# Kernel tuning notes

Measured on AMD Instinct MI355X. Metric: run time of the kernel, lower is better.

The kernel has to match this reference:

```python
import jax, jax.numpy as jnp
import numpy as np

N_NODES = 100000
N_EDGES = 1600000
NFEAT = 256
NHID = 128


def _l2_normalize(v, eps=1e-12):
    return v / (jnp.linalg.norm(v) + eps)


def setup_inputs() -> dict:
    key = jax.random.key(0)
    k1, k2, k3, k4 = jax.random.split(key, 4)
    x = jax.random.normal(k1, (N_NODES, NFEAT), dtype=jnp.float32)
    edge_index = jax.random.randint(k2, (2, N_EDGES), 0, N_NODES, dtype=jnp.int64)
    # GCNConv weight (glorot-ish scale), spectral-normalized at forward time
    W = jax.random.normal(k3, (NFEAT, NHID), dtype=jnp.float32) * 0.05
    bias = jnp.zeros((NHID,), dtype=jnp.float32)
    prelu_a = jnp.full((1,), 0.25, dtype=jnp.float32)  # nn.PReLU default slope
    u = _l2_normalize(jax.random.normal(k4, (NFEAT,), dtype=jnp.float32))
    return {"x": x, "edge_index": edge_index, "W": W, "bias": bias,
            "prelu_a": prelu_a, "u": u}


def reference(x, edge_index, W, bias, prelu_a, u):
    # --- spectral_norm: one power iteration (torch default n_power_iterations=1) ---
    v = _l2_normalize(W.T @ u)          # [NHID]
    u2 = _l2_normalize(W @ v)           # [NFEAT]
    sigma = u2 @ (W @ v)
    W_sn = W / sigma

    # --- GCNConv: linear transform, add self-loops, sym-normalize, scatter-add ---
    xw = x @ W_sn                       # [N, NHID]
    n = x.shape[0]
    loops = jnp.arange(n, dtype=edge_index.dtype)
    row = jnp.concatenate([edge_index[0], loops])  # sources
    col = jnp.concatenate([edge_index[1], loops])  # targets
    ones = jnp.ones(row.shape[0], dtype=x.dtype)
    deg = jax.ops.segment_sum(ones, col, num_segments=n)
    dinv = jnp.where(deg > 0, deg ** -0.5, 0.0)
    norm = dinv[row] * dinv[col]        # [E+N]
    msgs = norm[:, None] * xw[row]      # gather at sources
    out = jax.ops.segment_sum(msgs, col, num_segments=n) + bias

    # --- PReLU ---
    return jnp.where(out > 0, out, prelu_a * out)
```

## Files before the change

### kernel.cpp

```cpp
#include <hip/hip_runtime.h>

#define NFEAT 256
#define NHID  128

#define NBK   391
#define EPB   4096
#define NBLK  391

typedef __bf16 bf16x8 __attribute__((ext_vector_type(8)));
typedef __bf16 bf16x4 __attribute__((ext_vector_type(4)));
typedef float  f32x4  __attribute__((ext_vector_type(4)));

__global__ __launch_bounds__(256) void sigma_kernel(const float* __restrict__ W,
                                                    const float* __restrict__ u,
                                                    float* __restrict__ scal) {
    __shared__ float v[NHID];
    __shared__ float red[256];
    int tid = threadIdx.x;

    float t = 0.f;
    if (tid < NHID) {
        for (int i = 0; i < NFEAT; ++i) t += W[i * NHID + tid] * u[i];
    }
    red[tid] = (tid < NHID) ? t * t : 0.f;
    __syncthreads();
    for (int s = 128; s > 0; s >>= 1) {
        if (tid < s) red[tid] += red[tid + s];
        __syncthreads();
    }
    float nv = sqrtf(red[0]);
    float inv_nv = 1.f / (nv + 1e-12f);
    __syncthreads();
    if (tid < NHID) v[tid] = t * inv_nv;
    __syncthreads();

    float wv = 0.f;
    for (int j = 0; j < NHID; ++j) wv += W[tid * NHID + j] * v[j];
    red[tid] = wv * wv;
    __syncthreads();
    for (int s = 128; s > 0; s >>= 1) {
        if (tid < s) red[tid] += red[tid + s];
        __syncthreads();
    }
    if (tid == 0) {
        float n2  = red[0];
        float nwv = sqrtf(n2);
        float sigma = n2 / (nwv + 1e-12f);
        scal[0] = 1.f / sigma;
    }
}

__global__ __launch_bounds__(256) void wt_kernel(const float* __restrict__ W,
                                                 const float* __restrict__ scal,
                                                 __bf16* __restrict__ WT) {
    int idx = blockIdx.x * 256 + threadIdx.x;
    int c = idx >> 8;
    int r = idx & 255;
    WT[c * NFEAT + r] = (__bf16)(W[r * NHID + c] * scal[0]);
}

__global__ __launch_bounds__(256) void hist_kernel(const int* __restrict__ ecol,
                                                   int* __restrict__ blkhist, int E) {
    __shared__ int hist[NBK];
    int tid = threadIdx.x, b = blockIdx.x;
    for (int k = tid; k < NBK; k += 256) hist[k] = 0;
    __syncthreads();
    int e0 = b * EPB;
#pragma unroll
    for (int j = 0; j < 16; ++j) {
        int idx = e0 + j * 256 + tid;
        if (idx < E) atomicAdd(&hist[ecol[idx] >> 8], 1);
    }
    __syncthreads();
    for (int k = tid; k < NBK; k += 256) blkhist[k * NBLK + b] = hist[k];
}

__global__ __launch_bounds__(256) void scan_rows_kernel(int* __restrict__ blkhist,
                                                        int* __restrict__ btot) {
    int k = blockIdx.x * 4 + (threadIdx.x >> 6);
    int lane = threadIdx.x & 63;
    if (k >= NBK) return;
    int carry = 0;
    for (int c0 = 0; c0 < NBLK; c0 += 64) {
        int b = c0 + lane;
        int v = (b < NBLK) ? blkhist[k * NBLK + b] : 0;
        int orig = v;
#pragma unroll
        for (int d = 1; d < 64; d <<= 1) {
            int t = __shfl_up(v, (unsigned)d, 64);
            if (lane >= d) v += t;
        }
        if (b < NBLK) blkhist[k * NBLK + b] = carry + v - orig;
        carry += __shfl(v, 63, 64);
    }
    if (lane == 0) btot[k] = carry;
}

__global__ __launch_bounds__(512) void scan_buckets_kernel(const int* __restrict__ btot,
                                                           int* __restrict__ bbase) {
    __shared__ int s[512];
    int tid = threadIdx.x;
    int v = (tid < NBK) ? btot[tid] : 0;
    s[tid] = v;
    __syncthreads();
    int val = v;
    for (int off = 1; off < 512; off <<= 1) {
        int t = (tid >= off) ? s[tid - off] : 0;
        __syncthreads();
        val += t;
        s[tid] = val;
        __syncthreads();
    }
    if (tid <= NBK) bbase[tid] = val - v;
}

__global__ __launch_bounds__(512) void coarse_scatter_kernel(const int* __restrict__ erow,
                                                             const int* __restrict__ ecol,
                                                             const int* __restrict__ blkhist,
                                                             const int* __restrict__ bbase,
                                                             unsigned int* __restrict__ rbuf,
                                                             int E) {
    __shared__ unsigned int rec[EPB];
    __shared__ unsigned short bk[EPB];
    __shared__ int hist[NBK], sc[512], lbase[NBK], lfill[NBK], gb[NBK];
    int tid = threadIdx.x, b = blockIdx.x;
    for (int k = tid; k < NBK; k += 512) { hist[k] = 0; lfill[k] = 0; }
    __syncthreads();
    int e0 = b * EPB;
    unsigned int rv[8];
    int kv[8];
#pragma unroll
    for (int j = 0; j < 8; ++j) {
        int idx = e0 + j * 512 + tid;
        if (idx < E) {
            int c = ecol[idx];
            int s = erow[idx];
            int k = c >> 8;
            kv[j] = k;
            rv[j] = ((unsigned int)(c & 255) << 24) | (unsigned int)s;
            atomicAdd(&hist[k], 1);
        } else kv[j] = -1;
    }
    __syncthreads();
    int hv = (tid < NBK) ? hist[tid] : 0;
    sc[tid] = hv;
    __syncthreads();
    int val = hv;
    for (int off = 1; off < 512; off <<= 1) {
        int t = (tid >= off) ? sc[tid - off] : 0;
        __syncthreads();
        val += t;
        sc[tid] = val;
        __syncthreads();
    }
    if (tid < NBK) {
        lbase[tid] = val - hv;
        gb[tid] = bbase[tid] + blkhist[tid * NBLK + b];
    }
    __syncthreads();
#pragma unroll
    for (int j = 0; j < 8; ++j) {
        if (kv[j] >= 0) {
            int p = lbase[kv[j]] + atomicAdd(&lfill[kv[j]], 1);
            rec[p] = rv[j];
            bk[p] = (unsigned short)kv[j];
        }
    }
    __syncthreads();
    int nval = E - e0;
    if (nval > EPB) nval = EPB;
    for (int p = tid; p < nval; p += 512) {
        int k = bk[p];
        rbuf[gb[k] + (p - lbase[k])] = rec[p];
    }
}

__global__ __launch_bounds__(256) void fine_kernel(const unsigned int* __restrict__ rbuf,
                                                   const int* __restrict__ bbase,
                                                   int* __restrict__ base_g,
                                                   int* __restrict__ cnt_g,
                                                   float* __restrict__ dinv,
                                                   int* __restrict__ ebuf, int n) {
    __shared__ int cnt[256], lb[256], lf[256], sc[256];
    int tid = threadIdx.x, k = blockIdx.x;
    int seg0 = bbase[k], seg1 = bbase[k + 1];
    cnt[tid] = 0;
    lf[tid] = 0;
    __syncthreads();
    for (int j = seg0 + tid; j < seg1; j += 256)
        atomicAdd(&cnt[rbuf[j] >> 24], 1);
    __syncthreads();
    int cv = cnt[tid];
    sc[tid] = cv;
    __syncthreads();
    int val = cv;
    for (int off = 1; off < 256; off <<= 1) {
        int t = (tid >= off) ? sc[tid - off] : 0;
        __syncthreads();
        val += t;
        sc[tid] = val;
        __syncthreads();
    }
    lb[tid] = val - cv;
    __syncthreads();
    int node = k * 256 + tid;
    if (node < n) {
        base_g[node] = seg0 + lb[tid];
        cnt_g[node] = cv;
        dinv[node] = rsqrtf((float)cv + 1.f);
    }
    for (int j = seg0 + tid; j < seg1; j += 256) {
        unsigned int r = rbuf[j];
        int dl = r >> 24;
        int p = seg0 + lb[dl] + atomicAdd(&lf[dl], 1);
        ebuf[p] = (int)(r & 0xFFFFFFu);
    }
}

__global__ __launch_bounds__(256) void gemm_mfma_kernel(const float* __restrict__ x,
                                                        const __bf16* __restrict__ WT,
                                                        const float* __restrict__ dinv,
                                                        __bf16* __restrict__ xwb, int nn) {
    int tid  = threadIdx.x;
    int lane = tid & 63;
    int w    = tid >> 6;
    int rfrag = lane & 15;
    int kg    = lane >> 4;
    int row0 = blockIdx.x * 64 + (w & 1) * 32;
    int col0 = (w >> 1) * 64;
    int r0 = row0 + rfrag;
    int r1 = r0 + 16;
    int lr0 = (r0 < nn) ? r0 : nn - 1;
    int lr1 = (r1 < nn) ? r1 : nn - 1;

    const float4* xr0 = (const float4*)(x + (size_t)lr0 * NFEAT);
    const float4* xr1 = (const float4*)(x + (size_t)lr1 * NFEAT);

    f32x4 acc0[4] = {};
    f32x4 acc1[4] = {};

    int idx0 = kg * 2;
    float4 a0 = xr0[idx0], b0 = xr0[idx0 + 1];
    float4 a1 = xr1[idx0], b1 = xr1[idx0 + 1];

#pragma unroll
    for (int ks = 0; ks < 8; ++ks) {
        bf16x8 af0, af1;
        af0[0] = (__bf16)a0.x; af0[1] = (__bf16)a0.y;
        af0[2] = (__bf16)a0.z; af0[3] = (__bf16)a0.w;
        af0[4] = (__bf16)b0.x; af0[5] = (__bf16)b0.y;
        af0[6] = (__bf16)b0.z; af0[7] = (__bf16)b0.w;
        af1[0] = (__bf16)a1.x; af1[1] = (__bf16)a1.y;
        af1[2] = (__bf16)a1.z; af1[3] = (__bf16)a1.w;
        af1[4] = (__bf16)b1.x; af1[5] = (__bf16)b1.y;
        af1[6] = (__bf16)b1.z; af1[7] = (__bf16)b1.w;

        if (ks < 7) {
            int nidx = (ks + 1) * 8 + kg * 2;
            a0 = xr0[nidx]; b0 = xr0[nidx + 1];
            a1 = xr1[nidx]; b1 = xr1[nidx + 1];
        }

        int koff = ks * 32 + kg * 8;
#pragma unroll
        for (int nt = 0; nt < 4; ++nt) {
            bf16x8 bf = *(const bf16x8*)&WT[(size_t)(col0 + nt * 16 + rfrag) * NFEAT + koff];
            acc0[nt] = __builtin_amdgcn_mfma_f32_16x16x32_bf16(bf, af0, acc0[nt], 0, 0, 0);
            acc1[nt] = __builtin_amdgcn_mfma_f32_16x16x32_bf16(bf, af1, acc1[nt], 0, 0, 0);
        }
    }

    if (r0 < nn) {
        float d = dinv[r0];
        __bf16* orow = xwb + (size_t)r0 * NHID + col0 + kg * 4;
#pragma unroll
        for (int nt = 0; nt < 4; ++nt) {
            bf16x4 v;
            v[0] = (__bf16)(acc0[nt][0] * d);
            v[1] = (__bf16)(acc0[nt][1] * d);
            v[2] = (__bf16)(acc0[nt][2] * d);
            v[3] = (__bf16)(acc0[nt][3] * d);
            *(bf16x4*)&orow[nt * 16] = v;
        }
    }
    if (r1 < nn) {
        float d = dinv[r1];
        __bf16* orow = xwb + (size_t)r1 * NHID + col0 + kg * 4;
#pragma unroll
        for (int nt = 0; nt < 4; ++nt) {
            bf16x4 v;
            v[0] = (__bf16)(acc1[nt][0] * d);
            v[1] = (__bf16)(acc1[nt][1] * d);
            v[2] = (__bf16)(acc1[nt][2] * d);
            v[3] = (__bf16)(acc1[nt][3] * d);
            *(bf16x4*)&orow[nt * 16] = v;
        }
    }
}

__global__ __launch_bounds__(256) void gather_kernel(const uint2* __restrict__ xb2,
                                                     const int* __restrict__ base,
                                                     const int* __restrict__ cnt,
                                                     const int* __restrict__ ebuf,
                                                     const float* __restrict__ dinv,
                                                     const float* __restrict__ bias,
                                                     const float* __restrict__ pa,
                                                     float* __restrict__ out, int n) {
    int tid = threadIdx.x;
    int sub = tid & 31;
    int node = (blockIdx.x * 256 + tid) >> 5;
    if (node >= n) return;

    int b = base[node];
    int deg = cnt[node];

    uint2 s0 = xb2[(size_t)node * 32 + sub];
    float a0 = __uint_as_float(s0.x << 16);
    float a1 = __uint_as_float(s0.x & 0xffff0000u);
    float a2 = __uint_as_float(s0.y << 16);
    float a3 = __uint_as_float(s0.y & 0xffff0000u);

    int k = 0;
    for (; k + 4 <= deg; k += 4) {
        int r0 = ebuf[b + k + 0];
        int r1 = ebuf[b + k + 1];
        int r2 = ebuf[b + k + 2];
        int r3 = ebuf[b + k + 3];
        uint2 v0 = xb2[(size_t)r0 * 32 + sub];
        uint2 v1 = xb2[(size_t)r1 * 32 + sub];
        uint2 v2 = xb2[(size_t)r2 * 32 + sub];
        uint2 v3 = xb2[(size_t)r3 * 32 + sub];
        a0 += __uint_as_float(v0.x << 16) + __uint_as_float(v1.x << 16)
            + __uint_as_float(v2.x << 16) + __uint_as_float(v3.x << 16);
        a1 += __uint_as_float(v0.x & 0xffff0000u) + __uint_as_float(v1.x & 0xffff0000u)
            + __uint_as_float(v2.x & 0xffff0000u) + __uint_as_float(v3.x & 0xffff0000u);
        a2 += __uint_as_float(v0.y << 16) + __uint_as_float(v1.y << 16)
            + __uint_as_float(v2.y << 16) + __uint_as_float(v3.y << 16);
        a3 += __uint_as_float(v0.y & 0xffff0000u) + __uint_as_float(v1.y & 0xffff0000u)
            + __uint_as_float(v2.y & 0xffff0000u) + __uint_as_float(v3.y & 0xffff0000u);
    }
    for (; k < deg; ++k) {
        int r = ebuf[b + k];
        uint2 v = xb2[(size_t)r * 32 + sub];
        a0 += __uint_as_float(v.x << 16);
        a1 += __uint_as_float(v.x & 0xffff0000u);
        a2 += __uint_as_float(v.y << 16);
        a3 += __uint_as_float(v.y & 0xffff0000u);
    }

    float s = dinv[node];
    float alpha = pa[0];
    float4 bb = ((const float4*)bias)[sub];
    float o0 = s * a0 + bb.x;
    float o1 = s * a1 + bb.y;
    float o2 = s * a2 + bb.z;
    float o3 = s * a3 + bb.w;
    o0 = o0 > 0.f ? o0 : alpha * o0;
    o1 = o1 > 0.f ? o1 : alpha * o1;
    o2 = o2 > 0.f ? o2 : alpha * o2;
    o3 = o3 > 0.f ? o3 : alpha * o3;
    ((float4*)out)[(size_t)node * 32 + sub] = make_float4(o0, o1, o2, o3);
}

extern "C" void kernel_launch(void* const* d_in, const int* in_sizes, int n_in,
                              void* d_out, int out_size, void* d_ws, size_t ws_size,
                              hipStream_t stream) {
    const float* x    = (const float*)d_in[0];
    const int*   ei   = (const int*)d_in[1];
    const float* W    = (const float*)d_in[2];
    const float* bias = (const float*)d_in[3];
    const float* pa   = (const float*)d_in[4];
    const float* u    = (const float*)d_in[5];

    int n = in_sizes[0] / NFEAT;
    int e = in_sizes[1] / 2;
    const int* erow = ei;
    const int* ecol = ei + e;

    float* out = (float*)d_out;
    char* ws = (char*)d_ws;
    float*        scal   = (float*)(ws);
    int*          btot   = (int*)  (ws + 0x0001000);
    int*          bbase  = (int*)  (ws + 0x0002000);
    __bf16*       WT     = (__bf16*)(ws + 0x0010000);
    int*          base_g = (int*)  (ws + 0x0100000);
    int*          cnt_g  = (int*)  (ws + 0x0200000);
    float*        dinv   = (float*)(ws + 0x0300000);
    int*          blkhist= (int*)  (ws + 0x0400000);
    unsigned int* rbuf   = (unsigned int*)(ws + 0x0500000);
    int*          ebuf   = (int*)  (ws + 0x0C00000);
    __bf16*       xwb    = (__bf16*)(ws + 0x1300000);

    sigma_kernel<<<1, 256, 0, stream>>>(W, u, scal);
    wt_kernel<<<(NFEAT * NHID) / 256, 256, 0, stream>>>(W, scal, WT);

    hist_kernel<<<NBLK, 256, 0, stream>>>(ecol, blkhist, e);
    scan_rows_kernel<<<(NBK + 3) / 4, 256, 0, stream>>>(blkhist, btot);
    scan_buckets_kernel<<<1, 512, 0, stream>>>(btot, bbase);
    coarse_scatter_kernel<<<NBLK, 512, 0, stream>>>(erow, ecol, blkhist, bbase, rbuf, e);
    fine_kernel<<<NBK, 256, 0, stream>>>(rbuf, bbase, base_g, cnt_g, dinv, ebuf, n);

    gemm_mfma_kernel<<<(n + 63) / 64, 256, 0, stream>>>(x, WT, dinv, xwb, n);

    long long gunits = (long long)n * 32;
    gather_kernel<<<(int)((gunits + 255) / 256), 256, 0, stream>>>(
        (const uint2*)xwb, base_g, cnt_g, ebuf, dinv, bias, pa, out, n);
}
```

Measured before the change: 174.7 us.

## Stage x tiles through swizzled double-buffered LDS in GEMM kernel

```diff
diff --git a/kernel.cpp b/kernel.cpp
--- a/kernel.cpp
+++ b/kernel.cpp
@@ -221,53 +221,79 @@
                                                         const __bf16* __restrict__ WT,
                                                         const float* __restrict__ dinv,
                                                         __bf16* __restrict__ xwb, int nn) {
+    __shared__ __bf16 xs[2][64][64];
+
     int tid  = threadIdx.x;
     int lane = tid & 63;
     int w    = tid >> 6;
     int rfrag = lane & 15;
     int kg    = lane >> 4;
-    int row0 = blockIdx.x * 64 + (w & 1) * 32;
+    int row0 = blockIdx.x * 64;
+
+    int srow = tid >> 2;
+    int sseg = tid & 3;
+    int gsrow = row0 + srow;
+    if (gsrow >= nn) gsrow = nn - 1;
+    const float4* sx = (const float4*)(x + (size_t)gsrow * NFEAT) + sseg * 4;
+    int sslot = sseg * 2;
+    int sr7 = srow & 7;
+
+    int crow0 = (w & 1) * 32 + rfrag;
     int col0 = (w >> 1) * 64;
-    int r0 = row0 + rfrag;
+    int r0 = row0 + crow0;
     int r1 = r0 + 16;
-    int lr0 = (r0 < nn) ? r0 : nn - 1;
-    int lr1 = (r1 < nn) ? r1 : nn - 1;
-
-    const float4* xr0 = (const float4*)(x + (size_t)lr0 * NFEAT);
-    const float4* xr1 = (const float4*)(x + (size_t)lr1 * NFEAT);
+    const __bf16* wb = WT + (size_t)(col0 + rfrag) * NFEAT + kg * 8;
+    int cr7 = crow0 & 7;
 
     f32x4 acc0[4] = {};
     f32x4 acc1[4] = {};
 
-    int idx0 = kg * 2;
-    float4 a0 = xr0[idx0], b0 = xr0[idx0 + 1];
-    float4 a1 = xr1[idx0], b1 = xr1[idx0 + 1];
-
-#pragma unroll
-    for (int ks = 0; ks < 8; ++ks) {
-        bf16x8 af0, af1;
-        af0[0] = (__bf16)a0.x; af0[1] = (__bf16)a0.y;
-        af0[2] = (__bf16)a0.z; af0[3] = (__bf16)a0.w;
-        af0[4] = (__bf16)b0.x; af0[5] = (__bf16)b0.y;
-        af0[6] = (__bf16)b0.z; af0[7] = (__bf16)b0.w;
-        af1[0] = (__bf16)a1.x; af1[1] = (__bf16)a1.y;
-        af1[2] = (__bf16)a1.z; af1[3] = (__bf16)a1.w;
-        af1[4] = (__bf16)b1.x; af1[5] = (__bf16)b1.y;
-        af1[6] = (__bf16)b1.z; af1[7] = (__bf16)b1.w;
-
-        if (ks < 7) {
-            int nidx = (ks + 1) * 8 + kg * 2;
-            a0 = xr0[nidx]; b0 = xr0[nidx + 1];
-            a1 = xr1[nidx]; b1 = xr1[nidx + 1];
-        }
-
-        int koff = ks * 32 + kg * 8;
-#pragma unroll
-        for (int nt = 0; nt < 4; ++nt) {
-            bf16x8 bf = *(const bf16x8*)&WT[(size_t)(col0 + nt * 16 + rfrag) * NFEAT + koff];
-            acc0[nt] = __builtin_amdgcn_mfma_f32_16x16x32_bf16(bf, af0, acc0[nt], 0, 0, 0);
-            acc1[nt] = __builtin_amdgcn_mfma_f32_16x16x32_bf16(bf, af1, acc1[nt], 0, 0, 0);
-        }
+    {
+        float4 f0 = sx[0], f1 = sx[1], f2 = sx[2], f3 = sx[3];
+        bf16x8 h0, h1;
+        h0[0] = (__bf16)f0.x; h0[1] = (__bf16)f0.y; h0[2] = (__bf16)f0.z; h0[3] = (__bf16)f0.w;
+        h0[4] = (__bf16)f1.x; h0[5] = (__bf16)f1.y; h0[6] = (__bf16)f1.z; h0[7] = (__bf16)f1.w;
+        h1[0] = (__bf16)f2.x; h1[1] = (__bf16)f2.y; h1[2] = (__bf16)f2.z; h1[3] = (__bf16)f2.w;
+        h1[4] = (__bf16)f3.x; h1[5] = (__bf16)f3.y; h1[6] = (__bf16)f3.z; h1[7] = (__bf16)f3.w;
+        *(bf16x8*)&xs[0][srow][(sslot ^ sr7) * 8]       = h0;
+        *(bf16x8*)&xs[0][srow][((sslot + 1) ^ sr7) * 8] = h1;
+    }
+    __syncthreads();
+
+#pragma unroll
+    for (int c = 0; c < 4; ++c) {
+        const int cur = c & 1;
+
+        float4 f0, f1, f2, f3;
+        if (c < 3) {
+            const float4* p = sx + (c + 1) * 16;
+            f0 = p[0]; f1 = p[1]; f2 = p[2]; f3 = p[3];
+        }
+
+#pragma unroll
+        for (int ks = 0; ks < 2; ++ks) {
+            int slog = ks * 4 + kg;
+            bf16x8 af0 = *(const bf16x8*)&xs[cur][crow0][(slog ^ cr7) * 8];
+            bf16x8 af1 = *(const bf16x8*)&xs[cur][crow0 + 16][(slog ^ cr7) * 8];
+            int koff = c * 64 + ks * 32;
+#pragma unroll
+            for (int nt = 0; nt < 4; ++nt) {
+                bf16x8 bf = *(const bf16x8*)(wb + (size_t)nt * 16 * NFEAT + koff);
+                acc0[nt] = __builtin_amdgcn_mfma_f32_16x16x32_bf16(bf, af0, acc0[nt], 0, 0, 0);
+                acc1[nt] = __builtin_amdgcn_mfma_f32_16x16x32_bf16(bf, af1, acc1[nt], 0, 0, 0);
+            }
+        }
+
+        if (c < 3) {
+            bf16x8 h0, h1;
+            h0[0] = (__bf16)f0.x; h0[1] = (__bf16)f0.y; h0[2] = (__bf16)f0.z; h0[3] = (__bf16)f0.w;
+            h0[4] = (__bf16)f1.x; h0[5] = (__bf16)f1.y; h0[6] = (__bf16)f1.z; h0[7] = (__bf16)f1.w;
+            h1[0] = (__bf16)f2.x; h1[1] = (__bf16)f2.y; h1[2] = (__bf16)f2.z; h1[3] = (__bf16)f2.w;
+            h1[4] = (__bf16)f3.x; h1[5] = (__bf16)f3.y; h1[6] = (__bf16)f3.z; h1[7] = (__bf16)f3.w;
+            *(bf16x8*)&xs[cur ^ 1][srow][(sslot ^ sr7) * 8]       = h0;
+            *(bf16x8*)&xs[cur ^ 1][srow][((sslot + 1) ^ sr7) * 8] = h1;
+        }
+        __syncthreads();
     }
 
     if (r0 < nn) {
```

Result: faster. 161.1 us (-7.8%).
